# Kernel optimization log

Hardware: AMD Instinct MI355X
Metric: run time of the kernel (lower is better)

Reference implementation:

```python
import jax, jax.numpy as jnp
import numpy as np

BS, P, D = 64, 300, 1024
NUM_CLASSES = 150


def setup_inputs() -> dict:
    key = jax.random.key(0)
    ks = jax.random.split(key, 12)
    s = 0.02
    return {
        "x": jax.random.normal(ks[0], (BS * P, D), jnp.float32),
        "subject": jax.random.normal(ks[1], (BS, D), jnp.float32),
        "obj": jax.random.normal(ks[2], (BS, D), jnp.float32),
        "relation": jax.random.normal(ks[3], (BS, D), jnp.float32),
        "W_theta": jax.random.normal(ks[4], (D, D), jnp.float32) * s,
        "b_theta": jax.random.normal(ks[5], (D,), jnp.float32) * s,
        "W_pair": jax.random.normal(ks[6], (3 * D, 1), jnp.float32) * s,
        "b_pair": jax.random.normal(ks[7], (1,), jnp.float32) * s,
        "W_cls": jax.random.normal(ks[8], (2 * D, 1), jnp.float32) * s,
        "b_cls": jax.random.normal(ks[9], (1,), jnp.float32) * s,
        "W_bbox": jax.random.normal(ks[10], (D, (NUM_CLASSES + 1) * 4), jnp.float32) * s,
        "b_bbox": jax.random.normal(ks[11], ((NUM_CLASSES + 1) * 4,), jnp.float32) * s,
    }


def reference(x, subject, obj, relation, W_theta, b_theta, W_pair, b_pair,
              W_cls, b_cls, W_bbox, b_bbox):
    bs = relation.shape[0]
    rel = relation @ W_theta + b_theta  # (bs, D)
    xb = x.reshape(bs, P, D)

    # cls_score_pair(concat([x1, x2, rel])) decomposed into 3 sliced matmuls.
    # x1[b,i,j] = x[b,j] (cols), x2[b,i,j] = x[b,i] (rows).
    Wa, Wb, Wc = W_pair[:D, 0], W_pair[D:2 * D, 0], W_pair[2 * D:, 0]
    col_term = xb @ Wa          # (bs, P) -> broadcast over rows i
    row_term = xb @ Wb          # (bs, P) -> broadcast over cols j
    rel_term = rel @ Wc + b_pair[0]  # (bs,)
    pair_score = jax.nn.sigmoid(row_term[:, :, None] + col_term[None if False else slice(None), None, :]
                                + rel_term[:, None, None])  # (bs, P, P)

    # cls_score on [x, subject] and [x, object]
    W1, W2 = W_cls[:D, 0], W_cls[D:, 0]
    xw = xb @ W1                                  # (bs, P)
    s_score = jax.nn.sigmoid(xw + (subject @ W2 + b_cls[0])[:, None])  # (bs, P)
    o_score = jax.nn.sigmoid(xw + (obj @ W2 + b_cls[0])[:, None])      # (bs, P)

    pair_score = pair_score * o_score[:, None, :] * s_score[:, :, None]

    x_subj = jnp.stack([1.0 - s_score, s_score], axis=-1).reshape(-1, 2)
    x_obj = jnp.stack([1.0 - o_score, o_score], axis=-1).reshape(-1, 2)

    bbox_deltas = x @ W_bbox + b_bbox  # (bs*P, (C+1)*4)
    return (x_subj, x_obj, pair_score, bbox_deltas)
```

## Files before the change

kernel.cpp:

```cpp
#include <hip/hip_runtime.h>

#define PP    300
#define DD    1024
#define NOUT  604
#define NROWS 19200
#define OFF_PAIR  76800
#define OFF_BBOX  5836800

typedef unsigned short u16;
typedef __attribute__((ext_vector_type(8))) short bf16x8;
typedef __attribute__((ext_vector_type(4))) float f32x4;

#define GLOBAL_AS __attribute__((address_space(1)))
#define LDS_AS    __attribute__((address_space(3)))

__device__ inline u16 f2bf(float f) {
    unsigned u = __float_as_uint(f);
    return (u16)((u + 0x7fffu + ((u >> 16) & 1u)) >> 16);
}
__device__ inline float dot4(float4 a, float4 b) {
    return fmaf(a.x, b.x, fmaf(a.y, b.y, fmaf(a.z, b.z, a.w * b.w)));
}
__device__ inline float sigmoidf(float z) { return 1.f / (1.f + __expf(-z)); }

__global__ void k_transpose(const float* __restrict__ W, u16* __restrict__ Bt) {
    __shared__ float tile[32][33];
    int k0 = blockIdx.x * 32;
    int n0 = blockIdx.y * 32;
    int tx = threadIdx.x;
    int ty = threadIdx.y;
#pragma unroll
    for (int i = 0; i < 4; ++i) {
        int k = k0 + ty + i * 8;
        int n = n0 + tx;
        tile[ty + i * 8][tx] = (n < NOUT) ? W[(size_t)k * NOUT + n] : 0.f;
    }
    __syncthreads();
#pragma unroll
    for (int i = 0; i < 4; ++i) {
        int n = n0 + ty + i * 8;
        int k = k0 + tx;
        Bt[(size_t)n * DD + k] = f2bf(tile[tx][ty + i * 8]);
    }
}

__global__ void k_vtheta(const float* __restrict__ Wt, const float* __restrict__ Wpair,
                         float* __restrict__ v) {
    int wave = threadIdx.x >> 6, lane = threadIdx.x & 63;
    int k = blockIdx.x * 4 + wave;
    const float4* row = (const float4*)(Wt + (size_t)k * DD);
    const float4* wc  = (const float4*)(Wpair + 2 * DD);
    float s = 0.f;
#pragma unroll
    for (int i = 0; i < 4; ++i) s += dot4(row[i * 64 + lane], wc[i * 64 + lane]);
#pragma unroll
    for (int off = 32; off; off >>= 1) s += __shfl_down(s, off, 64);
    if (lane == 0) v[k] = s;
}

__global__ void k_scalars(const float* __restrict__ relation, const float* __restrict__ subject,
                          const float* __restrict__ obj, const float* __restrict__ btheta,
                          const float* __restrict__ Wpair, const float* __restrict__ bpair,
                          const float* __restrict__ Wcls, const float* __restrict__ bcls,
                          const float* __restrict__ v,
                          float* __restrict__ relt, float* __restrict__ subc,
                          float* __restrict__ objc) {
    __shared__ float red[4];
    int wave = threadIdx.x >> 6, lane = threadIdx.x & 63;
    int b = blockIdx.x;
    const float4* aa;
    const float4* bb;
    if (wave == 0)      { aa = (const float4*)(relation + (size_t)b * DD); bb = (const float4*)v; }
    else if (wave == 1) { aa = (const float4*)(subject + (size_t)b * DD);  bb = (const float4*)(Wcls + DD); }
    else if (wave == 2) { aa = (const float4*)(obj + (size_t)b * DD);      bb = (const float4*)(Wcls + DD); }
    else                { aa = (const float4*)btheta;                      bb = (const float4*)(Wpair + 2 * DD); }
    float s = 0.f;
#pragma unroll
    for (int i = 0; i < 4; ++i) s += dot4(aa[i * 64 + lane], bb[i * 64 + lane]);
#pragma unroll
    for (int off = 32; off; off >>= 1) s += __shfl_down(s, off, 64);
    if (lane == 0) red[wave] = s;
    __syncthreads();
    if (threadIdx.x == 0) {
        relt[b] = red[0] + red[3] + bpair[0];
        subc[b] = red[1] + bcls[0];
        objc[b] = red[2] + bcls[0];
    }
}

__global__ __launch_bounds__(256) void k_rows(
        const float* __restrict__ x, const float* __restrict__ Wpair,
        const float* __restrict__ Wcls,
        const float* __restrict__ relt, const float* __restrict__ subc,
        const float* __restrict__ objc,
        float* __restrict__ colv, float* __restrict__ rowp,
        float* __restrict__ sarr, float* __restrict__ oarr,
        float* __restrict__ out) {
    int wave = threadIdx.x >> 6, lane = threadIdx.x & 63;
    int r = blockIdx.x * 4 + wave;
    const float4* xr = (const float4*)(x + (size_t)r * DD);
    const float4* wa = (const float4*)(Wpair);
    const float4* wb = (const float4*)(Wpair + DD);
    const float4* w1 = (const float4*)(Wcls);
    float ca = 0.f, cb = 0.f, cw = 0.f;
#pragma unroll
    for (int i = 0; i < 4; ++i) {
        int idx = i * 64 + lane;
        float4 xv = xr[idx];
        ca += dot4(xv, wa[idx]);
        cb += dot4(xv, wb[idx]);
        cw += dot4(xv, w1[idx]);
    }
#pragma unroll
    for (int off = 32; off; off >>= 1) {
        ca += __shfl_down(ca, off, 64);
        cb += __shfl_down(cb, off, 64);
        cw += __shfl_down(cw, off, 64);
    }
    if (lane == 0) {
        int b = r / 300;
        float s = sigmoidf(cw + subc[b]);
        float o = sigmoidf(cw + objc[b]);
        colv[r] = ca;
        rowp[r] = cb + relt[b];
        sarr[r] = s;
        oarr[r] = o;
        ((float2*)out)[r]         = make_float2(1.f - s, s);
        ((float2*)out)[NROWS + r] = make_float2(1.f - o, o);
    }
}

__global__ __launch_bounds__(192) void k_pair(
        const float* __restrict__ rowp, const float* __restrict__ colv,
        const float* __restrict__ sarr, const float* __restrict__ oarr,
        float* __restrict__ pout) {
    int r = blockIdx.x;
    int b = r / 300;
    int j = threadIdx.x;
    if (j >= 150) return;
    float rp = rowp[r];
    float ss = sarr[r];
    const float* cb = colv + b * 300;
    const float* ob = oarr + b * 300;
    float p0 = sigmoidf(rp + cb[2 * j])     * ob[2 * j]     * ss;
    float p1 = sigmoidf(rp + cb[2 * j + 1]) * ob[2 * j + 1] * ss;
    ((float2*)(pout + (size_t)r * 300))[j] = make_float2(p0, p1);
}

#define BKK 64
__global__ __launch_bounds__(256) void k_gemm(
        const float* __restrict__ x, const u16* __restrict__ bt,
        const float* __restrict__ bias, float* __restrict__ out) {
    __shared__ u16 As[128 * BKK] __attribute__((aligned(16)));
    __shared__ u16 Bs[128 * BKK] __attribute__((aligned(16)));

    int bid = blockIdx.x;
    int xcd = bid & 7;
    int rest = bid >> 3;
    int n_t = rest % 5;
    int m_t = (rest / 5) * 8 + xcd;
    if (m_t >= 150) return;

    int tid = threadIdx.x;
    int wave = tid >> 6;
    int lane = tid & 63;
    int wr = wave >> 1, wc = wave & 1;
    int quad = lane >> 4;
    int l16 = lane & 15;

    f32x4 acc[4][4] = {};

    const float* a_base = x  + (size_t)m_t * 128 * DD;
    const u16*   b_base = bt + (size_t)n_t * 128 * DD;
    int s_row = lane >> 3;
    int s_c16 = lane & 7;
    int arow8 = tid >> 4;
    int acol4 = tid & 15;

    for (int k0 = 0; k0 < DD; k0 += BKK) {
#pragma unroll
        for (int q = 0; q < 4; ++q) {
            int rowblk = q * 32 + wave * 8;
            const u16* gb = b_base + (size_t)(rowblk + s_row) * DD + k0 + s_c16 * 8;
            __builtin_amdgcn_global_load_lds((const GLOBAL_AS unsigned int*)gb,
                                             (LDS_AS unsigned int*)(Bs + rowblk * BKK),
                                             16, 0, 0);
        }
#pragma unroll
        for (int it = 0; it < 8; ++it) {
            int row = it * 16 + arow8;
            float4 av = *(const float4*)(a_base + (size_t)row * DD + k0 + acol4 * 4);
            unsigned lo = __builtin_amdgcn_perm(__float_as_uint(av.y), __float_as_uint(av.x), 0x07060302u);
            unsigned hi = __builtin_amdgcn_perm(__float_as_uint(av.w), __float_as_uint(av.z), 0x07060302u);
            *(uint2*)(As + row * BKK + acol4 * 4) = make_uint2(lo, hi);
        }
        __syncthreads();
#pragma unroll
        for (int kk = 0; kk < BKK; kk += 32) {
            bf16x8 af[4], bfv[4];
#pragma unroll
            for (int f = 0; f < 4; ++f) {
                int m = wr * 64 + f * 16 + l16;
                af[f] = *(const bf16x8*)(As + m * BKK + kk + quad * 8);
                int n = wc * 64 + f * 16 + l16;
                bfv[f] = *(const bf16x8*)(Bs + n * BKK + kk + quad * 8);
            }
#pragma unroll
            for (int fi = 0; fi < 4; ++fi)
#pragma unroll
                for (int fj = 0; fj < 4; ++fj)
                    acc[fi][fj] = __builtin_amdgcn_mfma_f32_16x16x32_bf16(
                        af[fi], bfv[fj], acc[fi][fj], 0, 0, 0);
        }
        __syncthreads();
    }

#pragma unroll
    for (int fj = 0; fj < 4; ++fj) {
        int col = n_t * 128 + wc * 64 + fj * 16 + l16;
        if (col < NOUT) {
            float bia = bias[col];
#pragma unroll
            for (int fi = 0; fi < 4; ++fi) {
#pragma unroll
                for (int rg = 0; rg < 4; ++rg) {
                    int row = m_t * 128 + wr * 64 + fi * 16 + quad * 4 + rg;
                    out[(size_t)row * NOUT + col] = acc[fi][fj][rg] + bia;
                }
            }
        }
    }
}

extern "C" void kernel_launch(void* const* d_in, const int* in_sizes, int n_in,
                              void* d_out, int out_size, void* d_ws, size_t ws_size,
                              hipStream_t stream) {
    const void* P[12] = {};
    int sv[3] = {-1, -1, -1}; int nsv = 0;
    int sc[2] = {-1, -1};     int nsc = 0;
    for (int i = 0; i < n_in; ++i) {
        switch (in_sizes[i]) {
            case 19660800: P[0]  = d_in[i]; break;
            case 65536:    if (nsv < 3) sv[nsv++] = i; break;
            case 1048576:  P[4]  = d_in[i]; break;
            case 1024:     P[5]  = d_in[i]; break;
            case 3072:     P[6]  = d_in[i]; break;
            case 1:        if (nsc < 2) sc[nsc++] = i; break;
            case 2048:     P[8]  = d_in[i]; break;
            case 618496:   P[10] = d_in[i]; break;
            case 604:      P[11] = d_in[i]; break;
            default: break;
        }
    }
    bool alpha = (n_in == 12 && in_sizes[0] == 618496);
    if (alpha) {
        P[2] = d_in[sv[0]]; P[3] = d_in[sv[1]]; P[1] = d_in[sv[2]];
        P[9] = d_in[sc[0]]; P[7] = d_in[sc[1]];
    } else {
        P[1] = d_in[sv[0]]; P[2] = d_in[sv[1]]; P[3] = d_in[sv[2]];
        P[7] = d_in[sc[0]]; P[9] = d_in[sc[1]];
    }
    const float* x        = (const float*)P[0];
    const float* subject  = (const float*)P[1];
    const float* obj      = (const float*)P[2];
    const float* relation = (const float*)P[3];
    const float* W_theta  = (const float*)P[4];
    const float* b_theta  = (const float*)P[5];
    const float* W_pair   = (const float*)P[6];
    const float* b_pair   = (const float*)P[7];
    const float* W_cls    = (const float*)P[8];
    const float* b_cls    = (const float*)P[9];
    const float* W_bbox   = (const float*)P[10];
    const float* b_bbox   = (const float*)P[11];
    float* out = (float*)d_out;

    char* ws = (char*)d_ws;
    float* v    = (float*)(ws + 0);
    float* relt = (float*)(ws + 4096);
    float* subc = (float*)(ws + 4352);
    float* objc = (float*)(ws + 4608);
    float* colv = (float*)(ws + 4864);
    float* rowp = (float*)(ws + 81664);
    float* sarr = (float*)(ws + 158464);
    float* oarr = (float*)(ws + 235264);
    u16*   Bt   = (u16*)(ws + 312064);

    k_transpose<<<dim3(32, 20), dim3(32, 8), 0, stream>>>(W_bbox, Bt);
    k_vtheta<<<256, 256, 0, stream>>>(W_theta, W_pair, v);
    k_scalars<<<64, 256, 0, stream>>>(relation, subject, obj, b_theta, W_pair, b_pair,
                                      W_cls, b_cls, v, relt, subc, objc);
    k_rows<<<4800, 256, 0, stream>>>(x, W_pair, W_cls, relt, subc, objc,
                                     colv, rowp, sarr, oarr, out);
    k_pair<<<19200, 192, 0, stream>>>(rowp, colv, sarr, oarr, out + OFF_PAIR);
    k_gemm<<<760, 256, 0, stream>>>(x, Bt, b_bbox, out + OFF_BBOX);
}
```

Measured before the change: 231.5 us.

## Double-buffer GEMM LDS with swizzle and batch pair-score rows per block

The bbox GEMM now prefetches the next K tile into registers while computing on the current tile, using two LDS buffers and an XOR swizzle to cut bank conflicts. The B operand now goes through registers instead of the direct global-to-LDS load. The pair-score kernel now processes 30 rows per block with column and obj vectors cached in shared memory, replacing one tiny block per row. The aim is to hide global-load latency, halve the barriers, and reduce launch and block overhead, at the cost of more registers and LDS per block.

```diff
diff --git a/kernel.cpp b/kernel.cpp
--- a/kernel.cpp
+++ b/kernel.cpp
@@ -10,9 +10,6 @@
 typedef unsigned short u16;
 typedef __attribute__((ext_vector_type(8))) short bf16x8;
 typedef __attribute__((ext_vector_type(4))) float f32x4;
-
-#define GLOBAL_AS __attribute__((address_space(1)))
-#define LDS_AS    __attribute__((address_space(3)))
 
 __device__ inline u16 f2bf(float f) {
     unsigned u = __float_as_uint(f);
@@ -130,29 +127,39 @@
     }
 }
 
-__global__ __launch_bounds__(192) void k_pair(
+__global__ __launch_bounds__(256) void k_pair(
         const float* __restrict__ rowp, const float* __restrict__ colv,
         const float* __restrict__ sarr, const float* __restrict__ oarr,
         float* __restrict__ pout) {
-    int r = blockIdx.x;
-    int b = r / 300;
-    int j = threadIdx.x;
-    if (j >= 150) return;
-    float rp = rowp[r];
-    float ss = sarr[r];
-    const float* cb = colv + b * 300;
-    const float* ob = oarr + b * 300;
-    float p0 = sigmoidf(rp + cb[2 * j])     * ob[2 * j]     * ss;
-    float p1 = sigmoidf(rp + cb[2 * j + 1]) * ob[2 * j + 1] * ss;
-    ((float2*)(pout + (size_t)r * 300))[j] = make_float2(p0, p1);
+    __shared__ float cbs[300], obs[300], rps[30], sss[30];
+    int b = blockIdx.x;
+    int i0 = blockIdx.y * 30;
+    int tid = threadIdx.x;
+    for (int t = tid; t < 300; t += 256) {
+        cbs[t] = colv[b * 300 + t];
+        obs[t] = oarr[b * 300 + t];
+    }
+    if (tid < 30) {
+        rps[tid] = rowp[b * 300 + i0 + tid];
+        sss[tid] = sarr[b * 300 + i0 + tid];
+    }
+    __syncthreads();
+    int wave = tid >> 6, lane = tid & 63;
+    for (int i = wave; i < 30; i += 4) {
+        float rp = rps[i], ss = sss[i];
+        size_t base = ((size_t)b * 300 + i0 + i) * 300;
+        for (int c = lane; c < 300; c += 64) {
+            pout[base + c] = sigmoidf(rp + cbs[c]) * obs[c] * ss;
+        }
+    }
 }
 
 #define BKK 64
 __global__ __launch_bounds__(256) void k_gemm(
         const float* __restrict__ x, const u16* __restrict__ bt,
         const float* __restrict__ bias, float* __restrict__ out) {
-    __shared__ u16 As[128 * BKK] __attribute__((aligned(16)));
-    __shared__ u16 Bs[128 * BKK] __attribute__((aligned(16)));
+    __shared__ u16 As[2][128 * BKK] __attribute__((aligned(16)));
+    __shared__ u16 Bs[2][128 * BKK] __attribute__((aligned(16)));
 
     int bid = blockIdx.x;
     int xcd = bid & 7;
@@ -170,49 +177,69 @@
 
     f32x4 acc[4][4] = {};
 
-    const float* a_base = x  + (size_t)m_t * 128 * DD;
-    const u16*   b_base = bt + (size_t)n_t * 128 * DD;
-    int s_row = lane >> 3;
-    int s_c16 = lane & 7;
-    int arow8 = tid >> 4;
-    int acol4 = tid & 15;
-
-    for (int k0 = 0; k0 < DD; k0 += BKK) {
-#pragma unroll
-        for (int q = 0; q < 4; ++q) {
-            int rowblk = q * 32 + wave * 8;
-            const u16* gb = b_base + (size_t)(rowblk + s_row) * DD + k0 + s_c16 * 8;
-            __builtin_amdgcn_global_load_lds((const GLOBAL_AS unsigned int*)gb,
-                                             (LDS_AS unsigned int*)(Bs + rowblk * BKK),
-                                             16, 0, 0);
+    int prow = tid >> 3;
+    int pc   = tid & 7;
+    int swz  = pc ^ (prow & 7);
+    const float* ap = x  + ((size_t)(m_t * 128 + prow)) * DD + pc * 8;
+    const u16*   bp = bt + ((size_t)(n_t * 128 + prow)) * DD + pc * 8;
+
+    float4 ar[4][2];
+    uint4  br[4];
+
+#define ISSUE_LOADS(K0)                                                   \
+    _Pragma("unroll")                                                     \
+    for (int it = 0; it < 4; ++it) {                                      \
+        const float* pa = ap + (size_t)(it * 32) * DD + (K0);             \
+        ar[it][0] = *(const float4*)(pa);                                 \
+        ar[it][1] = *(const float4*)(pa + 4);                             \
+        br[it]    = *(const uint4*)(bp + (size_t)(it * 32) * DD + (K0));  \
+    }
+
+#define WRITE_LDS(BUF)                                                    \
+    _Pragma("unroll")                                                     \
+    for (int it = 0; it < 4; ++it) {                                      \
+        int pch = (it * 32 + prow) * 8 + swz;                             \
+        unsigned c0 = __builtin_amdgcn_perm(__float_as_uint(ar[it][0].y), __float_as_uint(ar[it][0].x), 0x07060302u); \
+        unsigned c1 = __builtin_amdgcn_perm(__float_as_uint(ar[it][0].w), __float_as_uint(ar[it][0].z), 0x07060302u); \
+        unsigned c2 = __builtin_amdgcn_perm(__float_as_uint(ar[it][1].y), __float_as_uint(ar[it][1].x), 0x07060302u); \
+        unsigned c3 = __builtin_amdgcn_perm(__float_as_uint(ar[it][1].w), __float_as_uint(ar[it][1].z), 0x07060302u); \
+        *(uint4*)(As[BUF] + pch * 8) = make_uint4(c0, c1, c2, c3);        \
+        *(uint4*)(Bs[BUF] + pch * 8) = br[it];                            \
+    }
+
+#define COMPUTE(BUF)                                                      \
+    _Pragma("unroll")                                                     \
+    for (int kc = 0; kc < 2; ++kc) {                                      \
+        bf16x8 af[4], bfv[4];                                             \
+        int lc = quad + kc * 4;                                           \
+        _Pragma("unroll")                                                 \
+        for (int f = 0; f < 4; ++f) {                                     \
+            int m = wr * 64 + f * 16 + l16;                               \
+            af[f]  = *(const bf16x8*)(As[BUF] + (m * 8 + (lc ^ (l16 & 7))) * 8); \
+            int n = wc * 64 + f * 16 + l16;                               \
+            bfv[f] = *(const bf16x8*)(Bs[BUF] + (n * 8 + (lc ^ (l16 & 7))) * 8); \
+        }                                                                 \
+        _Pragma("unroll")                                                 \
+        for (int fi = 0; fi < 4; ++fi)                                    \
+            _Pragma("unroll")                                             \
+            for (int fj = 0; fj < 4; ++fj)                                \
+                acc[fi][fj] = __builtin_amdgcn_mfma_f32_16x16x32_bf16(    \
+                    af[fi], bfv[fj], acc[fi][fj], 0, 0, 0);               \
+    }
+
+    ISSUE_LOADS(0);
+    WRITE_LDS(0);
+    __syncthreads();
+
+    int buf = 0;
+    for (int k0 = BKK; k0 <= DD; k0 += BKK) {
+        if (k0 < DD) { ISSUE_LOADS(k0); }
+        COMPUTE(buf);
+        if (k0 < DD) {
+            WRITE_LDS(buf ^ 1);
+            __syncthreads();
+            buf ^= 1;
         }
-#pragma unroll
-        for (int it = 0; it < 8; ++it) {
-            int row = it * 16 + arow8;
-            float4 av = *(const float4*)(a_base + (size_t)row * DD + k0 + acol4 * 4);
-            unsigned lo = __builtin_amdgcn_perm(__float_as_uint(av.y), __float_as_uint(av.x), 0x07060302u);
-            unsigned hi = __builtin_amdgcn_perm(__float_as_uint(av.w), __float_as_uint(av.z), 0x07060302u);
-            *(uint2*)(As + row * BKK + acol4 * 4) = make_uint2(lo, hi);
-        }
-        __syncthreads();
-#pragma unroll
-        for (int kk = 0; kk < BKK; kk += 32) {
-            bf16x8 af[4], bfv[4];
-#pragma unroll
-            for (int f = 0; f < 4; ++f) {
-                int m = wr * 64 + f * 16 + l16;
-                af[f] = *(const bf16x8*)(As + m * BKK + kk + quad * 8);
-                int n = wc * 64 + f * 16 + l16;
-                bfv[f] = *(const bf16x8*)(Bs + n * BKK + kk + quad * 8);
-            }
-#pragma unroll
-            for (int fi = 0; fi < 4; ++fi)
-#pragma unroll
-                for (int fj = 0; fj < 4; ++fj)
-                    acc[fi][fj] = __builtin_amdgcn_mfma_f32_16x16x32_bf16(
-                        af[fi], bfv[fj], acc[fi][fj], 0, 0, 0);
-        }
-        __syncthreads();
     }
 
 #pragma unroll
@@ -230,6 +257,9 @@
             }
         }
     }
+#undef ISSUE_LOADS
+#undef WRITE_LDS
+#undef COMPUTE
 }
 
 extern "C" void kernel_launch(void* const* d_in, const int* in_sizes, int n_in,
@@ -291,6 +321,6 @@
                                       W_cls, b_cls, v, relt, subc, objc);
     k_rows<<<4800, 256, 0, stream>>>(x, W_pair, W_cls, relt, subc, objc,
                                      colv, rowp, sarr, oarr, out);
-    k_pair<<<19200, 192, 0, stream>>>(rowp, colv, sarr, oarr, out + OFF_PAIR);
+    k_pair<<<dim3(64, 10), 256, 0, stream>>>(rowp, colv, sarr, oarr, out + OFF_PAIR);
     k_gemm<<<760, 256, 0, stream>>>(x, Bt, b_bbox, out + OFF_BBOX);
 }
```

New measurement: 244.6 us. 5.7% more time.
